# Optimization experiments

Measured on AMD Instinct MI355X. Metric: run time of the kernel, lower is better.

The kernel has to match this reference:

```python
import jax, jax.numpy as jnp
import numpy as np

B, S, H = 4, 4096, 4096
E, G, TOPK_GROUP, TOP_K = 160, 8, 3, 6
SCALE = 16.0      # routed_scaling_factor (norm_topk_prob=False)
ALPHA = 0.001     # aux_loss_alpha
M = 3             # config.M for communication aux loss


def setup_inputs() -> dict:
    key = jax.random.key(0)
    k1, k2 = jax.random.split(key)
    hidden_states = jax.random.normal(k1, (B, S, H), dtype=jnp.float32)
    # kaiming_uniform_(a=sqrt(5)) on (E, H): bound = 1/sqrt(fan_in)
    bound = 1.0 / np.sqrt(H)
    weight = jax.random.uniform(k2, (E, H), minval=-bound, maxval=bound, dtype=jnp.float32)
    return {"hidden_states": hidden_states, "weight": weight}


def _gate(hidden_states, weight):
    b, s, h = hidden_states.shape
    x = hidden_states.reshape(-1, h).astype(jnp.float32)          # [T, H]
    logits = x @ weight.astype(jnp.float32).T                      # [T, E]
    scores = jax.nn.softmax(logits, axis=-1)
    T = b * s
    # group-limited greedy top-k
    group_scores = scores.reshape(T, G, E // G).max(axis=-1)       # [T, G]
    _, group_idx = jax.lax.top_k(group_scores, TOPK_GROUP)         # [T, topk_group]
    group_mask = jnp.zeros((T, G), scores.dtype).at[
        jnp.arange(T)[:, None], group_idx].set(1.0)                # [T, G]
    score_mask = jnp.repeat(group_mask, E // G, axis=1)            # [T, E]
    tmp_scores = jnp.where(score_mask > 0, scores, 0.0)
    topk_weight, topk_idx = jax.lax.top_k(tmp_scores, TOP_K)       # [T, k]
    topk_weight = topk_weight * SCALE
    # --- aux losses (training, seq_aux=True, alpha>0) ---
    idx_flat = topk_idx.reshape(b, s * TOP_K)                      # [b, s*k]
    counts = jax.vmap(
        lambda idx: jnp.zeros((E,), jnp.float32).at[idx].add(1.0)
    )(idx_flat)                                                    # [b, E]
    ce = counts / (s * TOP_K / E)
    mean_scores = scores.reshape(b, s, E).mean(axis=1)             # [b, E]
    aux_expert = (ce * mean_scores).sum(axis=1).mean() * ALPHA
    ce_g = ce.reshape(b, G, -1).mean(axis=-1)                      # [b, G]
    ms_g = mean_scores.reshape(b, G, -1).mean(axis=-1)             # [b, G]
    aux_device = (ce_g * ms_g).sum(axis=1).mean() * ALPHA
    ce2 = counts.reshape(b, G, -1).sum(axis=-1) / (M * s / G)      # [b, G]
    aux_comm = (ce2 * ms_g).sum(axis=1).mean() * ALPHA
    aux_loss = aux_expert + aux_device + aux_comm
    return topk_idx, topk_weight, aux_loss


def reference(hidden_states, weight):
    return _gate(hidden_states, weight)
```

## Files before the change

kernel.cpp:

```cpp
#include <hip/hip_runtime.h>

typedef _Float16 half8 __attribute__((ext_vector_type(8)));
typedef float f32x4 __attribute__((ext_vector_type(4)));

#define H    4096
#define NE   160
#define BM   32
#define TPB  512
#define NIT  64


__global__ __launch_bounds__(256) void prep_kernel(
    const float* __restrict__ w, _Float16* __restrict__ Wf)
{
    int F    = blockIdx.x * 256 + threadIdx.x;
    int lane = F & 63;
    int t10  = (F >> 6) % 10;
    int ks   = F / 640;
    int e    = t10 * 16 + (lane & 15);
    int k0   = ks * 32 + (lane >> 4) * 8;
    const float* p = w + (size_t)e * H + k0;
    float4 v0 = *(const float4*)p;
    float4 v1 = *(const float4*)(p + 4);
    float vv[8] = {v0.x, v0.y, v0.z, v0.w, v1.x, v1.y, v1.z, v1.w};
    half8 h0, h1;
#pragma unroll
    for (int j = 0; j < 8; ++j) {
        float s = vv[j] * 64.f;
        _Float16 a = (_Float16)s;
        h0[j] = a;
        h1[j] = (_Float16)((s - (float)a) * 2048.f);
    }
    half8* out = (half8*)Wf;
    out[(ks * 20 + t10) * 64 + lane]      = h0;
    out[(ks * 20 + 10 + t10) * 64 + lane] = h1;
}

#define GLOAD_LDS(SRC, DST)                                                    \
    __builtin_amdgcn_global_load_lds(                                          \
        (const __attribute__((address_space(1))) unsigned int*)(SRC),          \
        (__attribute__((address_space(3))) unsigned int*)(DST), 16, 0, 0)

#define CONVERT(U0, U1)                                                        \
    do {                                                                       \
        float v0=U0.x, v1=U0.y, v2=U0.z, v3=U0.w;                              \
        float v4=U1.x, v5=U1.y, v6=U1.z, v7=U1.w;                              \
        _Float16 h;                                                            \
        h=(_Float16)v0; a0[0]=h; a1[0]=(_Float16)((v0-(float)h)*2048.f);       \
        h=(_Float16)v1; a0[1]=h; a1[1]=(_Float16)((v1-(float)h)*2048.f);       \
        h=(_Float16)v2; a0[2]=h; a1[2]=(_Float16)((v2-(float)h)*2048.f);       \
        h=(_Float16)v3; a0[3]=h; a1[3]=(_Float16)((v3-(float)h)*2048.f);       \
        h=(_Float16)v4; a0[4]=h; a1[4]=(_Float16)((v4-(float)h)*2048.f);       \
        h=(_Float16)v5; a0[5]=h; a1[5]=(_Float16)((v5-(float)h)*2048.f);       \
        h=(_Float16)v6; a0[6]=h; a1[6]=(_Float16)((v6-(float)h)*2048.f);       \
        h=(_Float16)v7; a0[7]=h; a1[7]=(_Float16)((v7-(float)h)*2048.f);       \
    } while (0)

__global__ __launch_bounds__(TPB) void gate_kernel(
    const float* __restrict__ x, const _Float16* __restrict__ Wf,
    float* __restrict__ outIdx, float* __restrict__ outW,
    float* __restrict__ gcnt, float* __restrict__ gssum)
{
    __shared__ __align__(16) _Float16 s_stage[2560 * 8];
    __shared__ float s_mx[BM], s_inv[BM];
    __shared__ int   s_cnt[NE];
    float* s_log = (float*)s_stage;

    const int tid  = threadIdx.x;
    const int lane = tid & 63;
    const int wv   = tid >> 6;
    const int kh   = wv >> 2;
    const int mh   = (wv >> 1) & 1;
    const int nh   = wv & 1;
    const int row0 = blockIdx.x * BM;

    if (tid < NE) s_cnt[tid] = 0;

    f32x4 accH[5], accL[5];
#pragma unroll
    for (int t = 0; t < 5; ++t) { accH[t] = (f32x4){0,0,0,0}; accL[t] = (f32x4){0,0,0,0}; }

    const float* xp = x + (size_t)(row0 + mh * 16 + (lane & 15)) * H
                        + kh * 32 + (lane >> 4) * 8;
    const int sbase = kh * 1280 + nh * 320 + lane;

    for (int it = 0; it < NIT; ++it) {
        __syncthreads();

        {
            const _Float16* srcH = Wf + ((size_t)it * 2560 + tid) * 8;
            _Float16*       dstH = s_stage + (size_t)tid * 8;
#pragma unroll
            for (int i = 0; i < 5; ++i)
                GLOAD_LDS(srcH + i * 4096, dstH + i * 4096);
        }
        float4 u0 = *(const float4*)(xp + (size_t)it * 64);
        float4 u1 = *(const float4*)(xp + (size_t)it * 64 + 4);

        __syncthreads();

        const half8* B = (const half8*)s_stage + sbase;
        half8 b0[5], b1[5];
#pragma unroll
        for (int t = 0; t < 5; ++t) { b0[t] = B[t * 64]; b1[t] = B[640 + t * 64]; }

        half8 a0, a1;
        CONVERT(u0, u1);
#pragma unroll
        for (int t = 0; t < 5; ++t) {
            accH[t] = __builtin_amdgcn_mfma_f32_16x16x32_f16(a0, b0[t], accH[t], 0, 0, 0);
            accL[t] = __builtin_amdgcn_mfma_f32_16x16x32_f16(a1, b0[t], accL[t], 0, 0, 0);
            accL[t] = __builtin_amdgcn_mfma_f32_16x16x32_f16(a0, b1[t], accL[t], 0, 0, 0);
        }
    }

    __syncthreads();

    const int crow  = mh * 16 + (lane >> 4) * 4;
    const int ccol0 = nh * 80 + (lane & 15);
    if (kh == 0) {
#pragma unroll
        for (int t = 0; t < 5; ++t)
#pragma unroll
            for (int r = 0; r < 4; ++r)
                s_log[(crow + r) * 161 + ccol0 + t * 16] =
                    (accH[t][r] + accL[t][r] * (1.0f / 2048.f)) * (1.0f / 64.f);
    }
    __syncthreads();
    if (kh == 1) {
#pragma unroll
        for (int t = 0; t < 5; ++t)
#pragma unroll
            for (int r = 0; r < 4; ++r)
                s_log[(crow + r) * 161 + ccol0 + t * 16] +=
                    (accH[t][r] + accL[t][r] * (1.0f / 2048.f)) * (1.0f / 64.f);
    }
    __syncthreads();

    if (tid < BM) {
        const float* L = &s_log[tid * 161];
        float gmax[8];
        float mx = -3.4e38f;
#pragma unroll
        for (int g = 0; g < 8; ++g) {
            float m = L[g * 20];
            for (int j = 1; j < 20; ++j) m = fmaxf(m, L[g * 20 + j]);
            gmax[g] = m;
            mx = fmaxf(mx, m);
        }
        float sum = 0.f;
        for (int e = 0; e < NE; ++e) sum += __expf(L[e] - mx);
        float inv = 1.0f / sum;
        s_mx[tid]  = mx;
        s_inv[tid] = inv;

        unsigned sel = 0;
        float pv = 3.4e38f; int pi = -1;
        for (int it = 0; it < 3; ++it) {
            float bv = -3.4e38f; int bi = 0;
            for (int g = 0; g < 8; ++g) {
                float v = gmax[g];
                bool below = (v < pv) || (v == pv && g > pi);
                if (below && v > bv) { bv = v; bi = g; }
            }
            sel |= 1u << bi;
            pv = bv; pi = bi;
        }

        const int tok = row0 + tid;
        float pv2 = 3.4e38f; int pi2 = -1;
        for (int it = 0; it < 6; ++it) {
            float bv = -3.4e38f; int bi = 0;
            for (int g = 0; g < 8; ++g) {
                if (!((sel >> g) & 1u)) continue;
                for (int j = 0; j < 20; ++j) {
                    int e = g * 20 + j;
                    float v = L[e];
                    bool below = (v < pv2) || (v == pv2 && e > pi2);
                    if (below && v > bv) { bv = v; bi = e; }
                }
            }
            pv2 = bv; pi2 = bi;
            outIdx[(size_t)tok * 6 + it] = (float)bi;
            outW[(size_t)tok * 6 + it]   = __expf(bv - mx) * inv * 16.0f;
            atomicAdd(&s_cnt[bi], 1);
        }
    }
    __syncthreads();

    if (tid < NE) {
        float ss = 0.f;
        for (int t2 = 0; t2 < BM; ++t2)
            ss += __expf(s_log[t2 * 161 + tid] - s_mx[t2]) * s_inv[t2];
        const int b = row0 >> 12;
        atomicAdd(&gssum[b * NE + tid], ss);
        atomicAdd(&gcnt[b * NE + tid], (float)s_cnt[tid]);
    }
}

__global__ __launch_bounds__(64) void aux_kernel(
    const float* __restrict__ gcnt, const float* __restrict__ gssum,
    float* __restrict__ out)
{
    const int lane = threadIdx.x;
    float part = 0.f;
    if (lane < 32) {
        const int b = lane >> 3, g = lane & 7;
        const float* cn = gcnt  + b * NE + g * 20;
        const float* sm = gssum + b * NE + g * 20;
        float s1 = 0.f, sc = 0.f, sms = 0.f;
        for (int j = 0; j < 20; ++j) {
            float ce = cn[j] * (1.0f / 153.6f);
            float ms = sm[j] * (1.0f / 4096.0f);
            s1  += ce * ms;
            sc  += cn[j];
            sms += ms;
        }
        float ceg = sc * (1.0f / 153.6f) * (1.0f / 20.0f);
        float msg = sms * (1.0f / 20.0f);
        float ce2 = sc * (1.0f / 1536.0f);
        part = s1 + ceg * msg + ce2 * msg;
    }
#pragma unroll
    for (int off = 32; off > 0; off >>= 1) part += __shfl_down(part, off);
    if (lane == 0) out[0] = part * (0.001f * 0.25f);
}

extern "C" void kernel_launch(void* const* d_in, const int* in_sizes, int n_in,
                              void* d_out, int out_size, void* d_ws, size_t ws_size,
                              hipStream_t stream)
{
    (void)in_sizes; (void)n_in; (void)out_size; (void)ws_size;
    const float* x = (const float*)d_in[0];
    const float* w = (const float*)d_in[1];
    float* out = (float*)d_out;

    _Float16* Wf  = (_Float16*)d_ws;
    float* gcnt  = (float*)(Wf + (size_t)NE * H * 2);
    float* gssum = gcnt + 4 * NE;

    hipMemsetAsync(gcnt, 0, 2 * 4 * NE * sizeof(float), stream);

    prep_kernel<<<(NE * H / 8) / 256, 256, 0, stream>>>(w, Wf);
    gate_kernel<<<16384 / BM, TPB, 0, stream>>>(
        x, Wf, out, out + 98304, gcnt, gssum);
    aux_kernel<<<1, 64, 0, stream>>>(gcnt, gssum, out + 196608);
}
```

Before: 242.4 us.

## Stage activation tiles into swizzled LDS via direct global-to-LDS loads

Activations were loaded straight from global memory into registers each iteration, 32 bytes per lane. They are now staged in 512-column chunks into LDS with an XOR swizzle, using bulk global-to-LDS loads, and the weight chunks are iterated inside each staged block. This aims for wider, more coalesced x loads and fewer stalls on global latency. In exchange LDS use grows a lot (64KB for x plus the weights and a separate logits buffer), which may cut occupancy. The x chunk is also consumed after only the weight barrier, relying on that barrier to cover the x load.

```diff
diff --git a/kernel.cpp b/kernel.cpp
--- a/kernel.cpp
+++ b/kernel.cpp
@@ -7,7 +7,8 @@
 #define NE   160
 #define BM   32
 #define TPB  512
-#define NIT  64
+#define NXT  8
+#define NWC  8
 
 
 __global__ __launch_bounds__(256) void prep_kernel(
@@ -61,10 +62,11 @@
     float* __restrict__ outIdx, float* __restrict__ outW,
     float* __restrict__ gcnt, float* __restrict__ gssum)
 {
-    __shared__ __align__(16) _Float16 s_stage[2560 * 8];
+    __shared__ __align__(16) float    s_x[BM * 512];
+    __shared__ __align__(16) _Float16 s_w[2560 * 8];
+    __shared__ float s_log[BM * 161];
     __shared__ float s_mx[BM], s_inv[BM];
     __shared__ int   s_cnt[NE];
-    float* s_log = (float*)s_stage;
 
     const int tid  = threadIdx.x;
     const int lane = tid & 63;
@@ -80,40 +82,55 @@
 #pragma unroll
     for (int t = 0; t < 5; ++t) { accH[t] = (f32x4){0,0,0,0}; accL[t] = (f32x4){0,0,0,0}; }
 
-    const float* xp = x + (size_t)(row0 + mh * 16 + (lane & 15)) * H
-                        + kh * 32 + (lane >> 4) * 8;
+    const int arow  = mh * 16 + (lane & 15);
+    const int aswz  = (arow & 7) << 4;
     const int sbase = kh * 1280 + nh * 320 + lane;
-
-    for (int it = 0; it < NIT; ++it) {
+    const char* Ar  = (const char*)(s_x + arow * 512);
+
+    for (int xt = 0; xt < NXT; ++xt) {
         __syncthreads();
 
-        {
-            const _Float16* srcH = Wf + ((size_t)it * 2560 + tid) * 8;
-            _Float16*       dstH = s_stage + (size_t)tid * 8;
-#pragma unroll
-            for (int i = 0; i < 5; ++i)
-                GLOAD_LDS(srcH + i * 4096, dstH + i * 4096);
-        }
-        float4 u0 = *(const float4*)(xp + (size_t)it * 64);
-        float4 u1 = *(const float4*)(xp + (size_t)it * 64 + 4);
-
-        __syncthreads();
-
-        const half8* B = (const half8*)s_stage + sbase;
-        half8 b0[5], b1[5];
-#pragma unroll
-        for (int t = 0; t < 5; ++t) { b0[t] = B[t * 64]; b1[t] = B[640 + t * 64]; }
-
-        half8 a0, a1;
-        CONVERT(u0, u1);
-#pragma unroll
-        for (int t = 0; t < 5; ++t) {
-            accH[t] = __builtin_amdgcn_mfma_f32_16x16x32_f16(a0, b0[t], accH[t], 0, 0, 0);
-            accL[t] = __builtin_amdgcn_mfma_f32_16x16x32_f16(a1, b0[t], accL[t], 0, 0, 0);
-            accL[t] = __builtin_amdgcn_mfma_f32_16x16x32_f16(a0, b1[t], accL[t], 0, 0, 0);
-        }
-    }
-
+#pragma unroll
+        for (int rd = 0; rd < 8; ++rd) {
+            int ii  = rd * 512 + tid;
+            int row = ii >> 7;
+            int c16 = ii & 127;
+            const float* src = x + (size_t)(row0 + row) * H + xt * 512
+                               + ((c16 ^ (row & 7)) << 2);
+            GLOAD_LDS(src, s_x + ii * 4);
+        }
+
+        for (int wc = 0; wc < NWC; ++wc) {
+            if (wc) __syncthreads();
+
+            {
+                const _Float16* src = Wf + ((size_t)(xt * NWC + wc) * 2560 + tid) * 8;
+                _Float16*       dst = s_w + (size_t)tid * 8;
+#pragma unroll
+                for (int i = 0; i < 5; ++i)
+                    GLOAD_LDS(src + i * 4096, dst + i * 4096);
+            }
+            __syncthreads();
+
+            const int acolb = (wc * 2 + kh) * 128 + (lane >> 4) * 32;
+            float4 u0 = *(const float4*)(Ar + ((acolb)      ^ aswz));
+            float4 u1 = *(const float4*)(Ar + ((acolb + 16) ^ aswz));
+
+            const half8* B = (const half8*)s_w + sbase;
+            half8 b0[5], b1[5];
+#pragma unroll
+            for (int t = 0; t < 5; ++t) { b0[t] = B[t * 64]; b1[t] = B[640 + t * 64]; }
+
+            half8 a0, a1;
+            CONVERT(u0, u1);
+#pragma unroll
+            for (int t = 0; t < 5; ++t) {
+                accH[t] = __builtin_amdgcn_mfma_f32_16x16x32_f16(a0, b0[t], accH[t], 0, 0, 0);
+                accL[t] = __builtin_amdgcn_mfma_f32_16x16x32_f16(a1, b0[t], accL[t], 0, 0, 0);
+                accL[t] = __builtin_amdgcn_mfma_f32_16x16x32_f16(a0, b1[t], accL[t], 0, 0, 0);
+            }
+        }
+    }
     __syncthreads();
 
     const int crow  = mh * 16 + (lane >> 4) * 4;
```

Measured after the change: 367.2 us. +51.5%, slower.

## Double-buffer W and x tiles in LDS with larger row blocks

Applied to the files above, without the earlier changes.

Doubles the row tile to 64 and the block to 1024 threads. Both the fp16 weight slices and the fp32 activation slices are now staged into LDS with global_load_lds in a two-stage ping-pong, so the next k-slice loads while the current one feeds the MFMAs. The activation tile gets an XOR swizzle to avoid LDS bank conflicts. This hides global-load latency and halves weight re-reads per row, at the cost of about 114KB of LDS per block, which caps occupancy at one block per CU.

```diff
diff --git a/kernel.cpp b/kernel.cpp
--- a/kernel.cpp
+++ b/kernel.cpp
@@ -5,8 +5,8 @@
 
 #define H    4096
 #define NE   160
-#define BM   32
-#define TPB  512
+#define BM   64
+#define TPB  1024
 #define NIT  64
 
 
@@ -41,6 +41,23 @@
         (const __attribute__((address_space(1))) unsigned int*)(SRC),          \
         (__attribute__((address_space(3))) unsigned int*)(DST), 16, 0, 0)
 
+#define STAGE_W(ITN, WOFF)                                                     \
+    do {                                                                       \
+        const _Float16* _s = Wf + ((size_t)(ITN) * 2560 + tid) * 8;            \
+        GLOAD_LDS(_s,            s_w + (WOFF) + (size_t)tid * 8);              \
+        GLOAD_LDS(_s + 8192,     s_w + (WOFF) + (size_t)(tid + 1024) * 8);     \
+        if (tid < 512)                                                         \
+            GLOAD_LDS(_s + 16384, s_w + (WOFF) + (size_t)(tid + 2048) * 8);    \
+    } while (0)
+
+#define STAGE_X(ITN, XOFF)                                                     \
+    do {                                                                       \
+        int _row = tid >> 4, _ch = tid & 15;                                   \
+        const float* _s = x + (size_t)(row0 + _row) * H + (ITN) * 64           \
+                          + ((_ch ^ (_row & 7)) << 2);                         \
+        GLOAD_LDS(_s, s_x + (XOFF) + tid * 4);                                 \
+    } while (0)
+
 #define CONVERT(U0, U1)                                                        \
     do {                                                                       \
         float v0=U0.x, v1=U0.y, v2=U0.z, v3=U0.w;                              \
@@ -56,21 +73,44 @@
         h=(_Float16)v7; a0[7]=h; a1[7]=(_Float16)((v7-(float)h)*2048.f);       \
     } while (0)
 
+#define COMPUTE(WOFF, XOFF)                                                    \
+    do {                                                                       \
+        const float* _xr = s_x + (XOFF) + arow * 64;                           \
+        float4 u0 = *(const float4*)(_xr + ((ch0 ^ r7) << 2));                 \
+        float4 u1 = *(const float4*)(_xr + ((ch1 ^ r7) << 2));                 \
+        const half8* B = (const half8*)(s_w + (WOFF)) + sbase;                 \
+        half8 b0[5], b1[5];                                                    \
+        _Pragma("unroll")                                                      \
+        for (int _t = 0; _t < 5; ++_t) {                                       \
+            b0[_t] = B[_t * 64];                                               \
+            b1[_t] = B[640 + _t * 64];                                         \
+        }                                                                      \
+        half8 a0, a1;                                                          \
+        CONVERT(u0, u1);                                                       \
+        _Pragma("unroll")                                                      \
+        for (int _t = 0; _t < 5; ++_t) {                                       \
+            accH[_t] = __builtin_amdgcn_mfma_f32_16x16x32_f16(a0, b0[_t], accH[_t], 0, 0, 0); \
+            accL[_t] = __builtin_amdgcn_mfma_f32_16x16x32_f16(a1, b0[_t], accL[_t], 0, 0, 0); \
+            accL[_t] = __builtin_amdgcn_mfma_f32_16x16x32_f16(a0, b1[_t], accL[_t], 0, 0, 0); \
+        }                                                                      \
+    } while (0)
+
 __global__ __launch_bounds__(TPB) void gate_kernel(
     const float* __restrict__ x, const _Float16* __restrict__ Wf,
     float* __restrict__ outIdx, float* __restrict__ outW,
     float* __restrict__ gcnt, float* __restrict__ gssum)
 {
-    __shared__ __align__(16) _Float16 s_stage[2560 * 8];
+    __shared__ __align__(16) _Float16 s_w[2 * 2560 * 8];
+    __shared__ __align__(16) float    s_x[2 * 4096];
     __shared__ float s_mx[BM], s_inv[BM];
     __shared__ int   s_cnt[NE];
-    float* s_log = (float*)s_stage;
+    float* s_log = (float*)s_w;
 
     const int tid  = threadIdx.x;
     const int lane = tid & 63;
     const int wv   = tid >> 6;
-    const int kh   = wv >> 2;
-    const int mh   = (wv >> 1) & 1;
+    const int kh   = wv >> 3;
+    const int mh   = (wv >> 1) & 3;
     const int nh   = wv & 1;
     const int row0 = blockIdx.x * BM;
 
@@ -80,41 +120,25 @@
 #pragma unroll
     for (int t = 0; t < 5; ++t) { accH[t] = (f32x4){0,0,0,0}; accL[t] = (f32x4){0,0,0,0}; }
 
-    const float* xp = x + (size_t)(row0 + mh * 16 + (lane & 15)) * H
-                        + kh * 32 + (lane >> 4) * 8;
     const int sbase = kh * 1280 + nh * 320 + lane;
-
-    for (int it = 0; it < NIT; ++it) {
+    const int arow  = mh * 16 + (lane & 15);
+    const int r7    = arow & 7;
+    const int ch0   = kh * 8 + (lane >> 4) * 2;
+    const int ch1   = ch0 + 1;
+
+    STAGE_W(0, 0);
+    STAGE_X(0, 0);
+    __syncthreads();
+
+    for (int it = 0; it < NIT; it += 2) {
+        if (it + 1 < NIT) { STAGE_W(it + 1, 20480); STAGE_X(it + 1, 4096); }
+        COMPUTE(0, 0);
         __syncthreads();
 
-        {
-            const _Float16* srcH = Wf + ((size_t)it * 2560 + tid) * 8;
-            _Float16*       dstH = s_stage + (size_t)tid * 8;
-#pragma unroll
-            for (int i = 0; i < 5; ++i)
-                GLOAD_LDS(srcH + i * 4096, dstH + i * 4096);
-        }
-        float4 u0 = *(const float4*)(xp + (size_t)it * 64);
-        float4 u1 = *(const float4*)(xp + (size_t)it * 64 + 4);
-
+        if (it + 2 < NIT) { STAGE_W(it + 2, 0); STAGE_X(it + 2, 0); }
+        COMPUTE(20480, 4096);
         __syncthreads();
-
-        const half8* B = (const half8*)s_stage + sbase;
-        half8 b0[5], b1[5];
-#pragma unroll
-        for (int t = 0; t < 5; ++t) { b0[t] = B[t * 64]; b1[t] = B[640 + t * 64]; }
-
-        half8 a0, a1;
-        CONVERT(u0, u1);
-#pragma unroll
-        for (int t = 0; t < 5; ++t) {
-            accH[t] = __builtin_amdgcn_mfma_f32_16x16x32_f16(a0, b0[t], accH[t], 0, 0, 0);
-            accL[t] = __builtin_amdgcn_mfma_f32_16x16x32_f16(a1, b0[t], accL[t], 0, 0, 0);
-            accL[t] = __builtin_amdgcn_mfma_f32_16x16x32_f16(a0, b1[t], accL[t], 0, 0, 0);
-        }
-    }
-
-    __syncthreads();
+    }
 
     const int crow  = mh * 16 + (lane >> 4) * 4;
     const int ccol0 = nh * 80 + (lane & 15);
```

Measured after the change: 195.5 us. -19.3%, faster.
